# Kernel tuning notes

Measured on AMD Instinct MI355X. Metric: run time of the kernel, lower is better.

The kernel has to match this reference:

```python
import jax, jax.numpy as jnp
import numpy as np

N = 4096      # number of stocks (token axis)
D = 512       # d_model
H = 8         # nhead
DE = 64       # d_emb
DH = D // H   # head_dim = 64
TEMP = float(np.sqrt(DH))
EPS = 1e-5


def _ln(x, g, b):
    mu = jnp.mean(x, axis=-1, keepdims=True)
    var = jnp.var(x, axis=-1, keepdims=True)
    return (x - mu) * jax.lax.rsqrt(var + EPS) * g + b


def setup_inputs() -> dict:
    key = jax.random.key(0)
    ks = jax.random.split(key, 8)
    init = lambda k, shape, fan: (jax.random.normal(k, shape, jnp.float32) / np.sqrt(fan).astype(np.float32))
    return {
        "x": jax.random.normal(ks[0], (N, D), jnp.float32),
        "industry_emb": jax.random.normal(ks[1], (N, DE), jnp.float32),
        # projection weights stored as [in, out] so y = x @ W
        "Wq": init(ks[2], (D + DE, D), D + DE),
        "Wk": init(ks[3], (D + DE, D), D + DE),
        "Wv": init(ks[4], (D, D), D),
        "g1": jnp.ones((D,), jnp.float32), "b1": jnp.zeros((D,), jnp.float32),
        "g2": jnp.ones((DE,), jnp.float32), "b2": jnp.zeros((DE,), jnp.float32),
        "g3": jnp.ones((D,), jnp.float32), "b3": jnp.zeros((D,), jnp.float32),
        "W_ffn1": init(ks[5], (D, D), D), "b_ffn1": jnp.zeros((D,), jnp.float32),
        "W_ffn2": init(ks[6], (D, D), D), "b_ffn2": jnp.zeros((D,), jnp.float32),
    }


def reference(x, industry_emb, Wq, Wk, Wv, g1, b1, g2, b2, g3, b3,
              W_ffn1, b_ffn1, W_ffn2, b_ffn2):
    xn = _ln(x, g1, b1)                       # [N, D]
    en = _ln(industry_emb, g2, b2)            # [N, DE]
    qk_in = jnp.concatenate([xn, en], axis=-1)  # [N, D+DE]
    q = (qk_in @ Wq).reshape(N, H, DH)
    k = (qk_in @ Wk).reshape(N, H, DH)
    v = (xn @ Wv).reshape(N, H, DH)
    # batched multi-head attention (equivalent to the per-head torch loop)
    scores = jnp.einsum('nhd,mhd->hnm', q, k) / TEMP   # [H, N, N]
    attn = jax.nn.softmax(scores, axis=-1)
    att = jnp.einsum('hnm,mhd->nhd', attn, v).reshape(N, D)
    xt = xn + att
    h = _ln(xt, g3, b3)
    ffn = jax.nn.relu(h @ W_ffn1 + b_ffn1) @ W_ffn2 + b_ffn2
    return xt + ffn
```

## Files before the change

### kernel.cpp

```cpp
#include <hip/hip_runtime.h>

#define NTOK 4096
#define DMODEL 512
#define DEMB 64
#define DCAT 576
#define NHEAD 8
#define DHEAD 64
#define QSCALE 0.18033688011112042f

typedef float f32x4 __attribute__((ext_vector_type(4)));
typedef short s16x8 __attribute__((ext_vector_type(8)));
typedef unsigned short u16;
typedef u16 u16x4 __attribute__((ext_vector_type(4)));
typedef u16 u16x8 __attribute__((ext_vector_type(8)));
typedef unsigned int u32;

__device__ __forceinline__ u16 f2bf(float f) {
  union { float f; unsigned u; } v; v.f = f;
  unsigned r = v.u + 0x7fffu + ((v.u >> 16) & 1u);
  return (u16)(r >> 16);
}

__device__ __forceinline__ float bf2f(u16 u) {
  union { unsigned u; float f; } v; v.u = ((unsigned)u) << 16;
  return v.f;
}

__device__ __forceinline__ u32 cvtpk_bf16(float lo, float hi) {
  u32 r;
  asm("v_cvt_pk_bf16_f32 %0, %1, %2" : "=v"(r) : "v"(lo), "v"(hi));
  return r;
}

__device__ __forceinline__ void gload16(const void* g, void* lds) {
  __builtin_amdgcn_global_load_lds((const __attribute__((address_space(1))) u32*)g,
                                   (__attribute__((address_space(3))) u32*)lds, 16, 0, 0);
}

__global__ void wtrans_kernel(const float* __restrict__ Wq, const float* __restrict__ Wk,
                              const float* __restrict__ Wv, const float* __restrict__ Wf1,
                              const float* __restrict__ Wf2,
                              u16* __restrict__ Tqkv, u16* __restrict__ Tf1, u16* __restrict__ Tf2) {
  __shared__ float tile[64][65];
  int w = blockIdx.z;
  const float* src; u16* dst; int Ksrc, Kdst;
  if (w == 0)      { src = Wq;  dst = Tqkv;              Ksrc = 576; Kdst = 576; }
  else if (w == 1) { src = Wk;  dst = Tqkv + 512 * 576;  Ksrc = 576; Kdst = 576; }
  else if (w == 2) { src = Wv;  dst = Tqkv + 1024 * 576; Ksrc = 512; Kdst = 576; }
  else if (w == 3) { src = Wf1; dst = Tf1;               Ksrc = 512; Kdst = 512; }
  else             { src = Wf2; dst = Tf2;               Ksrc = 512; Kdst = 512; }
  int kb = blockIdx.x * 64;
  if (kb >= Kdst) return;
  int nb = blockIdx.y * 64;
  int tid = threadIdx.x;
  #pragma unroll
  for (int i = 0; i < 16; ++i) {
    int idx = tid + i * 256;
    int r = idx >> 6, c = idx & 63;
    tile[r][c] = (kb + r < Ksrc) ? src[(size_t)(kb + r) * DMODEL + nb + c] : 0.0f;
  }
  __syncthreads();
  #pragma unroll
  for (int i = 0; i < 16; ++i) {
    int idx = tid + i * 256;
    int r = idx >> 6, c = idx & 63;
    dst[(size_t)(nb + r) * Kdst + kb + c] = f2bf(tile[c][r]);
  }
}

__global__ void lnx_kernel(const float* __restrict__ x, const float* __restrict__ g,
                           const float* __restrict__ b, float* __restrict__ xt,
                           u16* __restrict__ qkin) {
  int row = blockIdx.x * 4 + (threadIdx.x >> 6);
  int lane = threadIdx.x & 63;
  const float* xr = x + (size_t)row * DMODEL + lane * 8;
  float v[8];
  float4 a0 = *(const float4*)xr;
  float4 a1 = *(const float4*)(xr + 4);
  v[0]=a0.x; v[1]=a0.y; v[2]=a0.z; v[3]=a0.w; v[4]=a1.x; v[5]=a1.y; v[6]=a1.z; v[7]=a1.w;
  float s = 0.f, ss = 0.f;
  #pragma unroll
  for (int j = 0; j < 8; ++j) { s += v[j]; ss += v[j]*v[j]; }
  #pragma unroll
  for (int off = 32; off > 0; off >>= 1) { s += __shfl_xor(s, off); ss += __shfl_xor(ss, off); }
  float mu = s * (1.0f / DMODEL);
  float var = ss * (1.0f / DMODEL) - mu * mu;
  float rs = rsqrtf(var + 1e-5f);
  float4 g0 = *(const float4*)(g + lane * 8);
  float4 g1v = *(const float4*)(g + lane * 8 + 4);
  float4 b0 = *(const float4*)(b + lane * 8);
  float4 b1v = *(const float4*)(b + lane * 8 + 4);
  float gg[8] = {g0.x,g0.y,g0.z,g0.w,g1v.x,g1v.y,g1v.z,g1v.w};
  float bb[8] = {b0.x,b0.y,b0.z,b0.w,b1v.x,b1v.y,b1v.z,b1v.w};
  float o[8]; u16x8 ob;
  #pragma unroll
  for (int j = 0; j < 8; ++j) { o[j] = (v[j]-mu)*rs*gg[j] + bb[j]; ob[j] = f2bf(o[j]); }
  float* xo = xt + (size_t)row * DMODEL + lane * 8;
  *(float4*)xo = make_float4(o[0],o[1],o[2],o[3]);
  *(float4*)(xo + 4) = make_float4(o[4],o[5],o[6],o[7]);
  *(u16x8*)(qkin + (size_t)row * DCAT + lane * 8) = ob;
}

__global__ void lne_kernel(const float* __restrict__ e, const float* __restrict__ g,
                           const float* __restrict__ b, u16* __restrict__ qkin) {
  int row = blockIdx.x * 4 + (threadIdx.x >> 6);
  int lane = threadIdx.x & 63;
  float v = e[(size_t)row * DEMB + lane];
  float s = v, ss = v * v;
  #pragma unroll
  for (int off = 32; off > 0; off >>= 1) { s += __shfl_xor(s, off); ss += __shfl_xor(ss, off); }
  float mu = s * (1.0f / DEMB);
  float var = ss * (1.0f / DEMB) - mu * mu;
  float rs = rsqrtf(var + 1e-5f);
  float o = (v - mu) * rs * g[lane] + b[lane];
  qkin[(size_t)row * DCAT + DMODEL + lane] = f2bf(o);
}

__global__ void ln3_kernel(float* __restrict__ xt, const float* __restrict__ g,
                           const float* __restrict__ b, u16* __restrict__ hb,
                           const u16* __restrict__ obuf, const float* __restrict__ lbuf) {
  int row = blockIdx.x * 4 + (threadIdx.x >> 6);
  int lane = threadIdx.x & 63;
  int h = lane >> 3;
  int dh0 = (lane & 7) * 8;
  float* xr = xt + (size_t)row * DMODEL + lane * 8;
  float v[8];
  float4 a0 = *(const float4*)xr;
  float4 a1 = *(const float4*)(xr + 4);
  v[0]=a0.x; v[1]=a0.y; v[2]=a0.z; v[3]=a0.w; v[4]=a1.x; v[5]=a1.y; v[6]=a1.z; v[7]=a1.w;
  float osum[8] = {};
  float lsum = 0.f;
  #pragma unroll
  for (int s = 0; s < 4; ++s) {
    size_t hb_idx = (size_t)(s * 8 + h) * NTOK + row;
    u16x8 ov = *(const u16x8*)(obuf + hb_idx * 64 + dh0);
    lsum += lbuf[hb_idx];
    #pragma unroll
    for (int j = 0; j < 8; ++j) osum[j] += bf2f(ov[j]);
  }
  float rcpl = 1.0f / lsum;
  #pragma unroll
  for (int j = 0; j < 8; ++j) v[j] += osum[j] * rcpl;
  *(float4*)xr = make_float4(v[0],v[1],v[2],v[3]);
  *(float4*)(xr + 4) = make_float4(v[4],v[5],v[6],v[7]);
  float s = 0.f, ss = 0.f;
  #pragma unroll
  for (int j = 0; j < 8; ++j) { s += v[j]; ss += v[j]*v[j]; }
  #pragma unroll
  for (int off = 32; off > 0; off >>= 1) { s += __shfl_xor(s, off); ss += __shfl_xor(ss, off); }
  float mu = s * (1.0f / DMODEL);
  float var = ss * (1.0f / DMODEL) - mu * mu;
  float rs = rsqrtf(var + 1e-5f);
  float4 g0 = *(const float4*)(g + lane * 8);
  float4 g1v = *(const float4*)(g + lane * 8 + 4);
  float4 b0 = *(const float4*)(b + lane * 8);
  float4 b1v = *(const float4*)(b + lane * 8 + 4);
  float gg[8] = {g0.x,g0.y,g0.z,g0.w,g1v.x,g1v.y,g1v.z,g1v.w};
  float bb[8] = {b0.x,b0.y,b0.z,b0.w,b1v.x,b1v.y,b1v.z,b1v.w};
  u16x8 ob;
  #pragma unroll
  for (int j = 0; j < 8; ++j) ob[j] = f2bf((v[j]-mu)*rs*gg[j] + bb[j]);
  *(u16x8*)(hb + (size_t)row * DMODEL + lane * 8) = ob;
}

template<int MODE>
__global__ __launch_bounds__(256) void gemm_kernel(
    const u16* __restrict__ A, int lda, const u16* __restrict__ Bt, int K,
    u16* __restrict__ outb, float* __restrict__ outf,
    const float* __restrict__ bias, const float* __restrict__ xt) {
  __shared__ __align__(16) u16 smem[8192];
  u16* Al = smem;
  u16* Bl = smem + 4096;
  int tid = threadIdx.x, lane = tid & 63, wid = tid >> 6;
  int li = lane & 15, g4 = lane >> 4;
  int n0 = blockIdx.x * 64, m0 = blockIdx.y * 64;
  int wr = (wid >> 1) * 32, wc = (wid & 1) * 32;
  f32x4 acc[2][2] = {};
  for (int k0 = 0; k0 < K; k0 += 64) {
    #pragma unroll
    for (int i = 0; i < 2; ++i) {
      int idx = i * 256 + tid;
      int row = idx >> 3, cb = (idx & 7) * 8;
      gload16(A + (size_t)(m0 + row) * lda + k0 + cb, (char*)Al + idx * 16);
    }
    #pragma unroll
    for (int i = 0; i < 2; ++i) {
      int idx = i * 256 + tid;
      int row = idx >> 3, cb = (idx & 7) * 8;
      gload16(Bt + (size_t)(n0 + row) * K + k0 + cb, (char*)Bl + idx * 16);
    }
    __syncthreads();
    #pragma unroll
    for (int kk = 0; kk < 2; ++kk) {
      s16x8 af[2], bfv[2];
      #pragma unroll
      for (int mi = 0; mi < 2; ++mi)
        af[mi] = *(const s16x8*)&Al[(wr + mi * 16 + li) * 64 + kk * 32 + g4 * 8];
      #pragma unroll
      for (int ni = 0; ni < 2; ++ni)
        bfv[ni] = *(const s16x8*)&Bl[(wc + ni * 16 + li) * 64 + kk * 32 + g4 * 8];
      #pragma unroll
      for (int mi = 0; mi < 2; ++mi)
        #pragma unroll
        for (int ni = 0; ni < 2; ++ni)
          acc[mi][ni] = __builtin_amdgcn_mfma_f32_16x16x32_bf16(af[mi], bfv[ni], acc[mi][ni], 0, 0, 0);
    }
    __syncthreads();
  }
  if (MODE == 0) {
    if (n0 < 1024) {
      float scale = (n0 < 512) ? QSCALE : 1.0f;
      int nb = (n0 < 512) ? n0 : n0 - 512;
      u16* dst = outb + ((n0 < 512) ? 0 : (size_t)NTOK * DMODEL);
      #pragma unroll
      for (int mi = 0; mi < 2; ++mi)
        #pragma unroll
        for (int ni = 0; ni < 2; ++ni) {
          int col = nb + wc + ni * 16 + li;
          int h = col >> 6, dh = col & 63;
          #pragma unroll
          for (int r = 0; r < 4; ++r) {
            int row = m0 + wr + mi * 16 + g4 * 4 + r;
            dst[((size_t)h * NTOK + row) * DHEAD + dh] = f2bf(acc[mi][ni][r] * scale);
          }
        }
    } else {
      u16* vT = outb + (size_t)2 * NTOK * DMODEL;
      u16* tp = smem;
      __syncthreads();
      #pragma unroll
      for (int mi = 0; mi < 2; ++mi)
        #pragma unroll
        for (int ni = 0; ni < 2; ++ni) {
          int cl = wc + ni * 16 + li;
          int r0 = wr + mi * 16 + g4 * 4;
          u16x4 pk;
          pk[0] = f2bf(acc[mi][ni][0]); pk[1] = f2bf(acc[mi][ni][1]);
          pk[2] = f2bf(acc[mi][ni][2]); pk[3] = f2bf(acc[mi][ni][3]);
          *(u16x4*)&tp[cl * 80 + r0] = pk;
        }
      __syncthreads();
      for (int c = tid; c < 512; c += 256) {
        int cl = c >> 3, seg = c & 7;
        u16x8 v = *(const u16x8*)&tp[cl * 80 + seg * 8];
        *(u16x8*)&vT[(size_t)(n0 - 1024 + cl) * NTOK + m0 + seg * 8] = v;
      }
    }
  } else {
    #pragma unroll
    for (int mi = 0; mi < 2; ++mi)
      #pragma unroll
      for (int ni = 0; ni < 2; ++ni) {
        int col = n0 + wc + ni * 16 + li;
        float bv = bias[col];
        #pragma unroll
        for (int r = 0; r < 4; ++r) {
          int row = m0 + wr + mi * 16 + g4 * 4 + r;
          float v = acc[mi][ni][r] + bv;
          if (MODE == 3) {
            v = fmaxf(v, 0.0f);
            outb[(size_t)row * DMODEL + col] = f2bf(v);
          } else {
            outf[(size_t)row * DMODEL + col] = v + xt[(size_t)row * DMODEL + col];
          }
        }
      }
  }
}

__global__ __launch_bounds__(256) void attn_kernel(
    const u16* __restrict__ qh, const u16* __restrict__ kh,
    const u16* __restrict__ vT, u16* __restrict__ obuf, float* __restrict__ lbuf) {
  __shared__ __align__(16) u16 kbuf[2][4096];
  __shared__ __align__(16) u16 vbuf[2][4096];
  __shared__ __align__(16) u16 p_lds[4][2048];
  int tid = threadIdx.x, lane = tid & 63, w = tid >> 6;
  int li = lane & 15, g4 = lane >> 4;
  int li7 = li & 7;
  int h = blockIdx.x & 7, ks = (blockIdx.x >> 3) & 3, qt = blockIdx.x >> 5;
  int q0w = qt * 128 + w * 32;
  int ko0 = ks * 1024;
  const u16* qbase = qh + ((size_t)h * NTOK + q0w) * DHEAD;
  s16x8 bq[2][2];
  #pragma unroll
  for (int mi = 0; mi < 2; ++mi)
    #pragma unroll
    for (int kk = 0; kk < 2; ++kk)
      bq[mi][kk] = *(const s16x8*)(qbase + (mi * 16 + li) * DHEAD + kk * 32 + g4 * 8);
  f32x4 o[2][4] = {};
  float l_run[2] = {0.f, 0.f};
  char* pw = (char*)&p_lds[w][0];
  const char* kh_b = (const char*)(kh + (size_t)h * NTOK * DHEAD);
  const char* v_b = (const char*)(vT + (size_t)h * DHEAD * NTOK);

  auto stage = [&](int c, int ko) {
    #pragma unroll
    for (int i = 0; i < 2; ++i) {
      int s = w * 128 + i * 64 + lane;
      int row = s >> 3;
      int cg = (s & 7) ^ (row & 7);
      gload16(kh_b + (size_t)(ko + row) * 128 + cg * 16,
              (char*)&kbuf[c][0] + (w * 128 + i * 64) * 16);
      gload16(v_b + (size_t)row * (NTOK * 2) + (size_t)ko * 2 + cg * 16,
              (char*)&vbuf[c][0] + (w * 128 + i * 64) * 16);
    }
  };

  stage(0, ko0);
  asm volatile("s_waitcnt vmcnt(0)" ::: "memory");
  __builtin_amdgcn_sched_barrier(0);
  __syncthreads();

  for (int t = 0; t < 16; ++t) {
    int cur = t & 1;
    if (t < 15) stage(cur ^ 1, ko0 + (t + 1) * 64);
    const u16* Kl = &kbuf[cur][0];
    const u16* Vl = &vbuf[cur][0];
    s16x8 ak[4][2];
    #pragma unroll
    for (int ni = 0; ni < 4; ++ni)
      #pragma unroll
      for (int kk = 0; kk < 2; ++kk)
        ak[ni][kk] = *(const s16x8*)&Kl[(ni * 16 + li) * 64 +
                                        (((kk * 64 + g4 * 16) ^ (li7 << 4)) >> 1)];
    #pragma unroll
    for (int mi = 0; mi < 2; ++mi) {
      f32x4 st[4];
      #pragma unroll
      for (int ni = 0; ni < 4; ++ni) {
        f32x4 z = {0.f, 0.f, 0.f, 0.f};
        z = __builtin_amdgcn_mfma_f32_16x16x32_bf16(ak[ni][0], bq[mi][0], z, 0, 0, 0);
        st[ni] = __builtin_amdgcn_mfma_f32_16x16x32_bf16(ak[ni][1], bq[mi][1], z, 0, 0, 0);
      }
      int rowoff = (mi * 16 + li) * 128;
      int swz = li7 << 4;
      float rs = 0.f;
      #pragma unroll
      for (int ni = 0; ni < 4; ++ni) {
        float p0 = __builtin_amdgcn_exp2f(st[ni][0]);
        float p1 = __builtin_amdgcn_exp2f(st[ni][1]);
        float p2 = __builtin_amdgcn_exp2f(st[ni][2]);
        float p3 = __builtin_amdgcn_exp2f(st[ni][3]);
        rs += (p0 + p1) + (p2 + p3);
        uint2 pk;
        pk.x = cvtpk_bf16(p0, p1);
        pk.y = cvtpk_bf16(p2, p3);
        *(uint2*)(pw + rowoff + (((ni * 16 + g4 * 4) * 2) ^ swz)) = pk;
      }
      l_run[mi] += rs;
    }
    #pragma unroll
    for (int ki = 0; ki < 2; ++ki) {
      s16x8 ap[2], bv[4];
      #pragma unroll
      for (int mi = 0; mi < 2; ++mi)
        ap[mi] = *(const s16x8*)(pw + (mi * 16 + li) * 128 +
                                 (((ki * 32 + g4 * 8) * 2) ^ (li7 << 4)));
      #pragma unroll
      for (int di = 0; di < 4; ++di)
        bv[di] = *(const s16x8*)&Vl[(di * 16 + li) * 64 +
                                    (((ki * 64 + g4 * 16) ^ (li7 << 4)) >> 1)];
      #pragma unroll
      for (int mi = 0; mi < 2; ++mi)
        #pragma unroll
        for (int di = 0; di < 4; ++di)
          o[mi][di] = __builtin_amdgcn_mfma_f32_16x16x32_bf16(ap[mi], bv[di], o[mi][di], 0, 0, 0);
    }
    if (t < 15) {
      asm volatile("s_waitcnt vmcnt(0)" ::: "memory");
      __builtin_amdgcn_sched_barrier(0);
    }
    __syncthreads();
  }

  size_t slice = (size_t)(ks * 8 + h) * NTOK;
  #pragma unroll
  for (int mi = 0; mi < 2; ++mi) {
    float v = l_run[mi];
    v += __shfl_xor(v, 16);
    v += __shfl_xor(v, 32);
    if (g4 == 0) lbuf[slice + q0w + mi * 16 + li] = v;
  }
  u16* ob = obuf + (slice + q0w) * 64;
  #pragma unroll
  for (int mi = 0; mi < 2; ++mi)
    #pragma unroll
    for (int di = 0; di < 4; ++di)
      #pragma unroll
      for (int r = 0; r < 4; ++r)
        ob[(size_t)(mi * 16 + g4 * 4 + r) * 64 + di * 16 + li] = f2bf(o[mi][di][r]);
}

extern "C" void kernel_launch(void* const* d_in, const int* in_sizes, int n_in,
                              void* d_out, int out_size, void* d_ws, size_t ws_size,
                              hipStream_t stream) {
  const float* x   = (const float*)d_in[0];
  const float* emb = (const float*)d_in[1];
  const float* Wq  = (const float*)d_in[2];
  const float* Wk  = (const float*)d_in[3];
  const float* Wv  = (const float*)d_in[4];
  const float* g1  = (const float*)d_in[5];
  const float* b1  = (const float*)d_in[6];
  const float* g2  = (const float*)d_in[7];
  const float* b2  = (const float*)d_in[8];
  const float* g3  = (const float*)d_in[9];
  const float* b3  = (const float*)d_in[10];
  const float* Wf1 = (const float*)d_in[11];
  const float* bf1 = (const float*)d_in[12];
  const float* Wf2 = (const float*)d_in[13];
  const float* bf2 = (const float*)d_in[14];
  float* out = (float*)d_out;

  char* ws = (char*)d_ws;
  size_t off = 0;
  auto alloc = [&](size_t bytes) { void* p = ws + off; off += (bytes + 255) & ~255ull; return p; };
  float* xt = (float*)alloc((size_t)NTOK * DMODEL * 4);
  u16* qkin = (u16*)alloc((size_t)NTOK * DCAT * 2);
  u16* hb   = (u16*)alloc((size_t)NTOK * DMODEL * 2);
  u16* r1   = (u16*)alloc((size_t)NTOK * DMODEL * 2);
  u16* qkvh = (u16*)alloc((size_t)3 * NTOK * DMODEL * 2);
  u16* Tqkv = (u16*)alloc((size_t)1536 * DCAT * 2);
  u16* Tf1  = (u16*)alloc((size_t)DMODEL * DMODEL * 2);
  u16* Tf2  = (u16*)alloc((size_t)DMODEL * DMODEL * 2);
  u16* obuf = (u16*)alloc((size_t)4 * NHEAD * NTOK * DHEAD * 2);
  float* lbuf = (float*)alloc((size_t)4 * NHEAD * NTOK * 4);
  u16* qhd = qkvh;
  u16* khd = qkvh + (size_t)NTOK * DMODEL;
  u16* vTd = qkvh + (size_t)2 * NTOK * DMODEL;

  wtrans_kernel<<<dim3(9, 8, 5), 256, 0, stream>>>(Wq, Wk, Wv, Wf1, Wf2, Tqkv, Tf1, Tf2);
  lnx_kernel<<<1024, 256, 0, stream>>>(x, g1, b1, xt, qkin);
  lne_kernel<<<1024, 256, 0, stream>>>(emb, g2, b2, qkin);
  gemm_kernel<0><<<dim3(24, 64), 256, 0, stream>>>(qkin, DCAT, Tqkv, DCAT, qkvh, nullptr, nullptr, nullptr);
  attn_kernel<<<1024, 256, 0, stream>>>(qhd, khd, vTd, obuf, lbuf);
  ln3_kernel<<<1024, 256, 0, stream>>>(xt, g3, b3, hb, obuf, lbuf);
  gemm_kernel<3><<<dim3(8, 64), 256, 0, stream>>>(hb, DMODEL, Tf1, DMODEL, r1, nullptr, bf1, nullptr);
  gemm_kernel<4><<<dim3(8, 64), 256, 0, stream>>>(r1, DMODEL, Tf2, DMODEL, nullptr, out, bf2, xt);
}
```

Baseline: 113.0 us.

## Rewrite attention inner loop with 32x32 MFMA keeping P in registers

The attention kernel moves from 16x16x32 to 32x32x16 bf16 MFMA tiles and computes scores transposed, so the exponentiated probabilities land in the register layout that the PV MFMA consumes as its A operand. This removes the per-wave P round trip through LDS and its shared buffer. K and V are staged in a transposed fragment-ordered LDS layout, and the V-transpose epilogue of the projection GEMM permutes row order to match the new fragment layout. The trailing barrier is skipped on the last iteration and launch bounds request 2 blocks per CU, which may increase register pressure.

```diff
diff --git a/kernel.cpp b/kernel.cpp
--- a/kernel.cpp
+++ b/kernel.cpp
@@ -9,6 +9,7 @@
 #define QSCALE 0.18033688011112042f
 
 typedef float f32x4 __attribute__((ext_vector_type(4)));
+typedef float f32x16 __attribute__((ext_vector_type(16)));
 typedef short s16x8 __attribute__((ext_vector_type(8)));
 typedef unsigned short u16;
 typedef u16 u16x4 __attribute__((ext_vector_type(4)));
@@ -234,10 +235,11 @@
         for (int ni = 0; ni < 2; ++ni) {
           int cl = wc + ni * 16 + li;
           int r0 = wr + mi * 16 + g4 * 4;
+          int r0p = (r0 & ~12) | ((r0 & 4) << 1) | ((r0 & 8) >> 1);
           u16x4 pk;
           pk[0] = f2bf(acc[mi][ni][0]); pk[1] = f2bf(acc[mi][ni][1]);
           pk[2] = f2bf(acc[mi][ni][2]); pk[3] = f2bf(acc[mi][ni][3]);
-          *(u16x4*)&tp[cl * 80 + r0] = pk;
+          *(u16x4*)&tp[cl * 80 + r0p] = pk;
         }
       __syncthreads();
       for (int c = tid; c < 512; c += 256) {
@@ -268,41 +270,34 @@
   }
 }
 
-__global__ __launch_bounds__(256) void attn_kernel(
+__global__ __launch_bounds__(256, 2) void attn_kernel(
     const u16* __restrict__ qh, const u16* __restrict__ kh,
     const u16* __restrict__ vT, u16* __restrict__ obuf, float* __restrict__ lbuf) {
-  __shared__ __align__(16) u16 kbuf[2][4096];
-  __shared__ __align__(16) u16 vbuf[2][4096];
-  __shared__ __align__(16) u16 p_lds[4][2048];
+  __shared__ __align__(16) u16 kbufT[2][4096];
+  __shared__ __align__(16) u16 vbufT[2][4096];
   int tid = threadIdx.x, lane = tid & 63, w = tid >> 6;
-  int li = lane & 15, g4 = lane >> 4;
-  int li7 = li & 7;
+  int lq = lane & 31, h5 = lane >> 5;
   int h = blockIdx.x & 7, ks = (blockIdx.x >> 3) & 3, qt = blockIdx.x >> 5;
   int q0w = qt * 128 + w * 32;
   int ko0 = ks * 1024;
-  const u16* qbase = qh + ((size_t)h * NTOK + q0w) * DHEAD;
-  s16x8 bq[2][2];
-  #pragma unroll
-  for (int mi = 0; mi < 2; ++mi)
-    #pragma unroll
-    for (int kk = 0; kk < 2; ++kk)
-      bq[mi][kk] = *(const s16x8*)(qbase + (mi * 16 + li) * DHEAD + kk * 32 + g4 * 8);
-  f32x4 o[2][4] = {};
-  float l_run[2] = {0.f, 0.f};
-  char* pw = (char*)&p_lds[w][0];
+  const u16* qb = qh + ((size_t)h * NTOK + q0w + lq) * DHEAD;
+  s16x8 qf[4];
+  #pragma unroll
+  for (int kc = 0; kc < 4; ++kc)
+    qf[kc] = *(const s16x8*)(qb + kc * 16 + h5 * 8);
+  f32x16 o[2] = {};
+  float lsum = 0.f;
   const char* kh_b = (const char*)(kh + (size_t)h * NTOK * DHEAD);
   const char* v_b = (const char*)(vT + (size_t)h * DHEAD * NTOK);
 
   auto stage = [&](int c, int ko) {
     #pragma unroll
     for (int i = 0; i < 2; ++i) {
-      int s = w * 128 + i * 64 + lane;
-      int row = s >> 3;
-      int cg = (s & 7) ^ (row & 7);
-      gload16(kh_b + (size_t)(ko + row) * 128 + cg * 16,
-              (char*)&kbuf[c][0] + (w * 128 + i * 64) * 16);
-      gload16(v_b + (size_t)row * (NTOK * 2) + (size_t)ko * 2 + cg * 16,
-              (char*)&vbuf[c][0] + (w * 128 + i * 64) * 16);
+      int s = tid + i * 256;
+      int lo6 = s & 63, r6 = s >> 6;
+      gload16(kh_b + (size_t)(ko + lo6) * 128 + r6 * 16, (char*)&kbufT[c][0] + s * 16);
+      gload16(v_b + (size_t)lo6 * (NTOK * 2) + (size_t)(ko + r6 * 8) * 2,
+              (char*)&vbufT[c][0] + s * 16);
     }
   };
 
@@ -314,81 +309,53 @@
   for (int t = 0; t < 16; ++t) {
     int cur = t & 1;
     if (t < 15) stage(cur ^ 1, ko0 + (t + 1) * 64);
-    const u16* Kl = &kbuf[cur][0];
-    const u16* Vl = &vbuf[cur][0];
-    s16x8 ak[4][2];
-    #pragma unroll
-    for (int ni = 0; ni < 4; ++ni)
-      #pragma unroll
-      for (int kk = 0; kk < 2; ++kk)
-        ak[ni][kk] = *(const s16x8*)&Kl[(ni * 16 + li) * 64 +
-                                        (((kk * 64 + g4 * 16) ^ (li7 << 4)) >> 1)];
-    #pragma unroll
-    for (int mi = 0; mi < 2; ++mi) {
-      f32x4 st[4];
-      #pragma unroll
-      for (int ni = 0; ni < 4; ++ni) {
-        f32x4 z = {0.f, 0.f, 0.f, 0.f};
-        z = __builtin_amdgcn_mfma_f32_16x16x32_bf16(ak[ni][0], bq[mi][0], z, 0, 0, 0);
-        st[ni] = __builtin_amdgcn_mfma_f32_16x16x32_bf16(ak[ni][1], bq[mi][1], z, 0, 0, 0);
+    const u16* Kl = &kbufT[cur][0];
+    const u16* Vl = &vbufT[cur][0];
+    #pragma unroll
+    for (int kb2 = 0; kb2 < 2; ++kb2) {
+      f32x16 st = {};
+      #pragma unroll
+      for (int kc = 0; kc < 4; ++kc) {
+        s16x8 kf = *(const s16x8*)(Kl + ((kc * 2 + h5) * 64 + kb2 * 32 + lq) * 8);
+        st = __builtin_amdgcn_mfma_f32_32x32x16_bf16(kf, qf[kc], st, 0, 0, 0);
       }
-      int rowoff = (mi * 16 + li) * 128;
-      int swz = li7 << 4;
-      float rs = 0.f;
-      #pragma unroll
-      for (int ni = 0; ni < 4; ++ni) {
-        float p0 = __builtin_amdgcn_exp2f(st[ni][0]);
-        float p1 = __builtin_amdgcn_exp2f(st[ni][1]);
-        float p2 = __builtin_amdgcn_exp2f(st[ni][2]);
-        float p3 = __builtin_amdgcn_exp2f(st[ni][3]);
-        rs += (p0 + p1) + (p2 + p3);
-        uint2 pk;
-        pk.x = cvtpk_bf16(p0, p1);
-        pk.y = cvtpk_bf16(p2, p3);
-        *(uint2*)(pw + rowoff + (((ni * 16 + g4 * 4) * 2) ^ swz)) = pk;
+      float p[16];
+      #pragma unroll
+      for (int r = 0; r < 16; ++r) { p[r] = __builtin_amdgcn_exp2f(st[r]); lsum += p[r]; }
+      #pragma unroll
+      for (int cl = 0; cl < 2; ++cl) {
+        int b = cl * 8;
+        union { u32 wv[4]; s16x8 hv; } pu;
+        pu.wv[0] = cvtpk_bf16(p[b + 0], p[b + 1]);
+        pu.wv[1] = cvtpk_bf16(p[b + 2], p[b + 3]);
+        pu.wv[2] = cvtpk_bf16(p[b + 4], p[b + 5]);
+        pu.wv[3] = cvtpk_bf16(p[b + 6], p[b + 7]);
+        int kcg = kb2 * 2 + cl;
+        #pragma unroll
+        for (int dhalf = 0; dhalf < 2; ++dhalf) {
+          s16x8 bv = *(const s16x8*)(Vl + ((kcg * 2 + h5) * 64 + dhalf * 32 + lq) * 8);
+          o[dhalf] = __builtin_amdgcn_mfma_f32_32x32x16_bf16(pu.hv, bv, o[dhalf], 0, 0, 0);
+        }
       }
-      l_run[mi] += rs;
-    }
-    #pragma unroll
-    for (int ki = 0; ki < 2; ++ki) {
-      s16x8 ap[2], bv[4];
-      #pragma unroll
-      for (int mi = 0; mi < 2; ++mi)
-        ap[mi] = *(const s16x8*)(pw + (mi * 16 + li) * 128 +
-                                 (((ki * 32 + g4 * 8) * 2) ^ (li7 << 4)));
-      #pragma unroll
-      for (int di = 0; di < 4; ++di)
-        bv[di] = *(const s16x8*)&Vl[(di * 16 + li) * 64 +
-                                    (((ki * 64 + g4 * 16) ^ (li7 << 4)) >> 1)];
-      #pragma unroll
-      for (int mi = 0; mi < 2; ++mi)
-        #pragma unroll
-        for (int di = 0; di < 4; ++di)
-          o[mi][di] = __builtin_amdgcn_mfma_f32_16x16x32_bf16(ap[mi], bv[di], o[mi][di], 0, 0, 0);
     }
     if (t < 15) {
       asm volatile("s_waitcnt vmcnt(0)" ::: "memory");
       __builtin_amdgcn_sched_barrier(0);
-    }
-    __syncthreads();
-  }
-
+      __syncthreads();
+    }
+  }
+
+  lsum += __shfl_xor(lsum, 32);
   size_t slice = (size_t)(ks * 8 + h) * NTOK;
-  #pragma unroll
-  for (int mi = 0; mi < 2; ++mi) {
-    float v = l_run[mi];
-    v += __shfl_xor(v, 16);
-    v += __shfl_xor(v, 32);
-    if (g4 == 0) lbuf[slice + q0w + mi * 16 + li] = v;
-  }
+  if (h5 == 0) lbuf[slice + q0w + lq] = lsum;
   u16* ob = obuf + (slice + q0w) * 64;
   #pragma unroll
-  for (int mi = 0; mi < 2; ++mi)
-    #pragma unroll
-    for (int di = 0; di < 4; ++di)
-      #pragma unroll
-      for (int r = 0; r < 4; ++r)
-        ob[(size_t)(mi * 16 + g4 * 4 + r) * 64 + di * 16 + li] = f2bf(o[mi][di][r]);
+  for (int dhalf = 0; dhalf < 2; ++dhalf)
+    #pragma unroll
+    for (int r = 0; r < 16; ++r) {
+      int crow = (r & 3) + 8 * (r >> 2) + 4 * h5;
+      ob[(size_t)crow * 64 + dhalf * 32 + lq] = f2bf(o[dhalf][r]);
+    }
 }
 
 extern "C" void kernel_launch(void* const* d_in, const int* in_sizes, int n_in,
```

Measured after the change: 110.7 us. 2.0% less time.
